# Performance work log

Hardware: AMD Instinct MI355X
Metric: run time of the kernel (lower is better)

Reference implementation:

```python
import jax, jax.numpy as jnp
import numpy as np
from jax import lax

D_VOCAB = 262
D_EMB = 128
CONV_W = 5
PAD = CONV_W // 2  # 2


def setup_inputs() -> dict:
    key = jax.random.key(0)
    k1, k2, k3, k4, k5 = jax.random.split(key, 5)
    B, W, C = 128, 256, 16
    input = jax.random.randint(k1, (B, W, C), 0, D_VOCAB, dtype=jnp.int64)
    lengths = jax.random.randint(k2, (B, W), 1, C + 1, dtype=jnp.int64)
    # torch init: Embedding weight ~ N(0,1) then *0.1
    emb_weight = jax.random.normal(k3, (D_VOCAB, D_EMB), dtype=jnp.float32) * 0.1
    fan_in = D_EMB * CONV_W
    bound = 1.0 / np.sqrt(fan_in)
    conv_w = jax.random.uniform(k4, (D_EMB, D_EMB, CONV_W), dtype=jnp.float32, minval=-bound, maxval=bound)
    conv_b = jax.random.uniform(k5, (D_EMB,), dtype=jnp.float32, minval=-bound, maxval=bound)
    return {"input": input, "lengths": lengths, "emb_weight": emb_weight,
            "conv_w": conv_w, "conv_b": conv_b}


def reference(input, lengths, emb_weight, conv_w, conv_b):
    B, W, C = input.shape
    ids = input.reshape(B * W, C)                      # [N, C]
    embed = emb_weight[ids]                            # [N, C, E] gather
    x = jnp.transpose(embed, (0, 2, 1))                # [N, E, C] (NCW)
    y = lax.conv_general_dilated(
        x, conv_w,
        window_strides=(1,), padding=[(PAD, PAD)],
        dimension_numbers=("NCH", "OIH", "NCH"))       # [N, E, C]
    y = y + conv_b[None, :, None]
    out = jnp.max(y, axis=-1)                          # max-pool over chars
    return out.reshape(B, W, -1)                       # [B, W, E]
```

## Files before the change

kernel.cpp:

```cpp
#include <hip/hip_runtime.h>
#include <hip/hip_fp16.h>

#define D_VOCAB 262
#define D_EMB   128
#define KW      5
#define NCHAR   16
#define NKO     (KW * D_EMB)

typedef _Float16 h8 __attribute__((ext_vector_type(8)));
typedef float    f8 __attribute__((ext_vector_type(8)));


__global__ __launch_bounds__(256) void transpose_w_kernel(
    const float* __restrict__ cw, float* __restrict__ Wt) {
  const int gid = blockIdx.x * 256 + threadIdx.x;
  const float val = cw[gid];
  const int o = gid / 640;
  const int r = gid - o * 640;
  const int i = r / 5;
  const int k = r - i * 5;
  Wt[(k * D_EMB + o) * D_EMB + i] = val;
}

__global__ __launch_bounds__(256) void compute_P_kernel(
    const float* __restrict__ emb, const float* __restrict__ Wt,
    _Float16* __restrict__ P) {
  const int wave = threadIdx.x >> 6;
  const int lane = threadIdx.x & 63;
  const int w = blockIdx.x * 4 + wave;
  const int v = w / 10;
  const int ko = (w - v * 10) * 64 + lane;

  const float* er = emb + v * D_EMB;
  const float4* wt = (const float4*)(Wt + ko * D_EMB);
  float acc = 0.f;
#pragma unroll 8
  for (int i4 = 0; i4 < 32; ++i4) {
    const float4 wv = wt[i4];
    acc += er[i4 * 4 + 0] * wv.x + er[i4 * 4 + 1] * wv.y +
           er[i4 * 4 + 2] * wv.z + er[i4 * 4 + 3] * wv.w;
  }
  P[v * NKO + ko] = (_Float16)acc;
}

__global__ __launch_bounds__(256) void conv_char_main_kernel(
    const int* __restrict__ ids, const _Float16* __restrict__ P,
    const float* __restrict__ bias, float* __restrict__ out) {
  const int lane = threadIdx.x & 63;
  const int wave = threadIdx.x >> 6;
  const int n_base = (blockIdx.x * 4 + wave) * 4;
  const int g4 = lane & 48;
  const int s = lane & 15;
  const int o = s * 8;
  const int n = n_base + (lane >> 4);

  const int myid = ids[n_base * NCHAR + lane];

  h8 win[5];
#pragma unroll
  for (int w = 0; w < 5; ++w) win[w] = (h8)(_Float16)0.f;
  h8 vmax = (h8)(_Float16)(-60000.f);

#pragma unroll
  for (int j = 0; j < NCHAR; ++j) {
    const int id = __shfl(myid, g4 + j);
    const _Float16* row = P + (size_t)id * NKO + o;
#pragma unroll
    for (int k = 0; k < KW; ++k) {
      const int c = j + 2 - k;
      if (c >= 0 && c < NCHAR) {
        const h8 val = *(const h8*)(row + k * D_EMB);
        win[c % 5] += val;
      }
    }
    if (j >= 2) {
      const int w = (j - 2) % 5;
      vmax = __builtin_elementwise_max(vmax, win[w]);
      win[w] = (h8)(_Float16)0.f;
    }
  }
  vmax = __builtin_elementwise_max(vmax, win[14 % 5]);
  vmax = __builtin_elementwise_max(vmax, win[15 % 5]);

  const f8 fv = __builtin_convertvector(vmax, f8);
  const f8 bv = *(const f8*)(bias + o);
  const f8 r = fv + bv;
  *(f8*)(out + (size_t)n * D_EMB + o) = r;
}

extern "C" void kernel_launch(void* const* d_in, const int* in_sizes, int n_in,
                              void* d_out, int out_size, void* d_ws, size_t ws_size,
                              hipStream_t stream) {
  const int*   input = (const int*)d_in[0];
  const float* emb   = (const float*)d_in[2];
  const float* cw    = (const float*)d_in[3];
  const float* cb    = (const float*)d_in[4];
  float* out = (float*)d_out;

  _Float16* P  = (_Float16*)d_ws;
  float*    Wt = (float*)((char*)d_ws + 335872);

  const int n_seq = in_sizes[0] / NCHAR;

  transpose_w_kernel<<<320, 256, 0, stream>>>(cw, Wt);
  compute_P_kernel<<<655, 256, 0, stream>>>(emb, Wt, P);

  const int blocks = n_seq / 16;
  conv_char_main_kernel<<<blocks, 256, 0, stream>>>(input, P, cb, out);
}
```

Measured before the change: 105.0 us.

## Stage channel-chunked projection table in LDS for the char-conv gather

The precomputed vocab×tap×channel projection table is re-laid out into 8 channel chunks of 16. Each 1024-thread block loads one chunk (about 42 KB, padded rows) into shared memory and handles 256 sequences for that chunk, so the per-character gathers hit LDS instead of global/L2. The cost is that every block reloads a chunk and the total work is split 8 ways by channel. The max is now accumulated in fp32 after half-precision window sums, and sequence bounds are checked.

```diff
diff --git a/kernel.cpp b/kernel.cpp
--- a/kernel.cpp
+++ b/kernel.cpp
@@ -5,10 +5,12 @@
 #define D_EMB   128
 #define KW      5
 #define NCHAR   16
-#define NKO     (KW * D_EMB)
-
-typedef _Float16 h8 __attribute__((ext_vector_type(8)));
-typedef float    f8 __attribute__((ext_vector_type(8)));
+#define NROW    (D_VOCAB * KW)
+#define CH      16
+#define NCHUNK  (D_EMB / CH)
+#define CHUNK_HALFS (NROW * CH)
+#define LROW2   10
+#define SEQ_PER_BLOCK 256
 
 
 __global__ __launch_bounds__(256) void transpose_w_kernel(
@@ -24,7 +26,7 @@
 
 __global__ __launch_bounds__(256) void compute_P_kernel(
     const float* __restrict__ emb, const float* __restrict__ Wt,
-    _Float16* __restrict__ P) {
+    __half* __restrict__ Pc) {
   const int wave = threadIdx.x >> 6;
   const int lane = threadIdx.x & 63;
   const int w = blockIdx.x * 4 + wave;
@@ -40,52 +42,89 @@
     acc += er[i4 * 4 + 0] * wv.x + er[i4 * 4 + 1] * wv.y +
            er[i4 * 4 + 2] * wv.z + er[i4 * 4 + 3] * wv.w;
   }
-  P[v * NKO + ko] = (_Float16)acc;
+  const int k = ko >> 7;
+  const int o = ko & 127;
+  Pc[(size_t)(o >> 4) * CHUNK_HALFS + (v * KW + k) * CH + (o & 15)] =
+      __float2half(acc);
 }
 
-__global__ __launch_bounds__(256) void conv_char_main_kernel(
-    const int* __restrict__ ids, const _Float16* __restrict__ P,
-    const float* __restrict__ bias, float* __restrict__ out) {
-  const int lane = threadIdx.x & 63;
-  const int wave = threadIdx.x >> 6;
-  const int n_base = (blockIdx.x * 4 + wave) * 4;
-  const int g4 = lane & 48;
-  const int s = lane & 15;
-  const int o = s * 8;
-  const int n = n_base + (lane >> 4);
+__global__ __launch_bounds__(1024, 8) void conv_char_main_kernel(
+    const int* __restrict__ ids, const __half* __restrict__ Pc,
+    const float* __restrict__ bias, float* __restrict__ out, int n_seq) {
+  __shared__ __half2 lds[NROW * LROW2];
 
-  const int myid = ids[n_base * NCHAR + lane];
+  const int t = threadIdx.x;
+  const int c = blockIdx.x & (NCHUNK - 1);
+  const int seqbase = (blockIdx.x >> 3) * SEQ_PER_BLOCK;
 
-  h8 win[5];
+  const int4* src = (const int4*)(Pc + (size_t)c * CHUNK_HALFS);
+  for (int t4 = t; t4 < CHUNK_HALFS / 8; t4 += 1024) {
+    const int4 v = src[t4];
+    const int row = t4 >> 1;
+    const int dst = row * LROW2 + (t4 & 1) * 4;
+    *(int2*)&lds[dst]     = make_int2(v.x, v.y);
+    *(int2*)&lds[dst + 2] = make_int2(v.z, v.w);
+  }
+  __syncthreads();
+
+  const int wave = t >> 6;
+  const int lane = t & 63;
+  const int q = lane & 3;
+  const int wseq = seqbase + wave * 16;
+  const int n = wseq + (lane >> 2);
+
+  int4 myids = make_int4(0, 0, 0, 0);
+  if (wseq + (lane >> 2) < n_seq)
+    myids = ((const int4*)(ids + (size_t)wseq * NCHAR))[lane];
+  const int ida[4] = {myids.x, myids.y, myids.z, myids.w};
+
+  const __half2 hz = __float2half2_rn(0.f);
+  __half2 win[5][2];
 #pragma unroll
-  for (int w = 0; w < 5; ++w) win[w] = (h8)(_Float16)0.f;
-  h8 vmax = (h8)(_Float16)(-60000.f);
+  for (int s = 0; s < 5; ++s) { win[s][0] = hz; win[s][1] = hz; }
+  float vmax[4] = {-1e30f, -1e30f, -1e30f, -1e30f};
 
 #pragma unroll
   for (int j = 0; j < NCHAR; ++j) {
-    const int id = __shfl(myid, g4 + j);
-    const _Float16* row = P + (size_t)id * NKO + o;
+    const int idv = __shfl(ida[j & 3], (lane & 60) + (j >> 2));
+    const __half2* rp = &lds[idv * (KW * LROW2) + q * 2];
 #pragma unroll
     for (int k = 0; k < KW; ++k) {
-      const int c = j + 2 - k;
-      if (c >= 0 && c < NCHAR) {
-        const h8 val = *(const h8*)(row + k * D_EMB);
-        win[c % 5] += val;
+      const int cc = j + 2 - k;
+      if (cc >= 0 && cc < NCHAR) {
+        const int2 rv = *(const int2*)(rp + k * LROW2);
+        const __half2 a = *(const __half2*)&rv.x;
+        const __half2 b = *(const __half2*)&rv.y;
+        __half2* ws = win[cc % 5];
+        ws[0] = __hadd2(ws[0], a);
+        ws[1] = __hadd2(ws[1], b);
       }
     }
     if (j >= 2) {
-      const int w = (j - 2) % 5;
-      vmax = __builtin_elementwise_max(vmax, win[w]);
-      win[w] = (h8)(_Float16)0.f;
+      const int s = (j - 2) % 5;
+      const float2 f0 = __half22float2(win[s][0]);
+      const float2 f1 = __half22float2(win[s][1]);
+      vmax[0] = fmaxf(vmax[0], f0.x); vmax[1] = fmaxf(vmax[1], f0.y);
+      vmax[2] = fmaxf(vmax[2], f1.x); vmax[3] = fmaxf(vmax[3], f1.y);
+      win[s][0] = hz; win[s][1] = hz;
     }
   }
-  vmax = __builtin_elementwise_max(vmax, win[14 % 5]);
-  vmax = __builtin_elementwise_max(vmax, win[15 % 5]);
+#pragma unroll
+  for (int cc = 14; cc < 16; ++cc) {
+    const int s = cc % 5;
+    const float2 f0 = __half22float2(win[s][0]);
+    const float2 f1 = __half22float2(win[s][1]);
+    vmax[0] = fmaxf(vmax[0], f0.x); vmax[1] = fmaxf(vmax[1], f0.y);
+    vmax[2] = fmaxf(vmax[2], f1.x); vmax[3] = fmaxf(vmax[3], f1.y);
+  }
 
-  const f8 fv = __builtin_convertvector(vmax, f8);
-  const f8 bv = *(const f8*)(bias + o);
-  const f8 r = fv + bv;
-  *(f8*)(out + (size_t)n * D_EMB + o) = r;
+  if (n < n_seq) {
+    const float4 bv = *(const float4*)(bias + c * CH + q * 4);
+    float4 r;
+    r.x = vmax[0] + bv.x; r.y = vmax[1] + bv.y;
+    r.z = vmax[2] + bv.z; r.w = vmax[3] + bv.w;
+    *(float4*)(out + (size_t)n * D_EMB + c * CH + q * 4) = r;
+  }
 }
 
 extern "C" void kernel_launch(void* const* d_in, const int* in_sizes, int n_in,
@@ -97,14 +136,15 @@
   const float* cb    = (const float*)d_in[4];
   float* out = (float*)d_out;
 
-  _Float16* P  = (_Float16*)d_ws;
-  float*    Wt = (float*)((char*)d_ws + 335872);
+  __half* Pc = (__half*)d_ws;
+  float*  Wt = (float*)((char*)d_ws + 335872);
 
   const int n_seq = in_sizes[0] / NCHAR;
 
   transpose_w_kernel<<<320, 256, 0, stream>>>(cw, Wt);
-  compute_P_kernel<<<655, 256, 0, stream>>>(emb, Wt, P);
+  compute_P_kernel<<<655, 256, 0, stream>>>(emb, Wt, Pc);
 
-  const int blocks = n_seq / 16;
-  conv_char_main_kernel<<<blocks, 256, 0, stream>>>(input, P, cb, out);
+  const int seq_blocks = (n_seq + SEQ_PER_BLOCK - 1) / SEQ_PER_BLOCK;
+  conv_char_main_kernel<<<seq_blocks * NCHUNK, 1024, 0, stream>>>(
+      input, Pc, cb, out, n_seq);
 }
```

After: 107.2 us. +2.2%, slower.

## Transpose conv weights to input-major layout and compute projection table per vocab row

Applied to the files above, without the earlier changes.

The conv weights are now transposed into an [i][k*E+o] layout, so each of the 640 threads in a block reads consecutive addresses when it loads one output column. Each vocab row gets one 640-thread block that stages its embedding vector in shared memory. This replaces strided per-thread float4 reads with coalesced loads across the wave. The precompute is small next to the main gather/conv kernel, so any gain is confined to that stage.

```diff
diff --git a/kernel.cpp b/kernel.cpp
--- a/kernel.cpp
+++ b/kernel.cpp
@@ -12,35 +12,31 @@
 
 
 __global__ __launch_bounds__(256) void transpose_w_kernel(
-    const float* __restrict__ cw, float* __restrict__ Wt) {
+    const float* __restrict__ cw, float* __restrict__ Wt2) {
   const int gid = blockIdx.x * 256 + threadIdx.x;
   const float val = cw[gid];
   const int o = gid / 640;
   const int r = gid - o * 640;
   const int i = r / 5;
   const int k = r - i * 5;
-  Wt[(k * D_EMB + o) * D_EMB + i] = val;
+  Wt2[i * NKO + k * D_EMB + o] = val;
 }
 
-__global__ __launch_bounds__(256) void compute_P_kernel(
-    const float* __restrict__ emb, const float* __restrict__ Wt,
-    _Float16* __restrict__ P) {
-  const int wave = threadIdx.x >> 6;
-  const int lane = threadIdx.x & 63;
-  const int w = blockIdx.x * 4 + wave;
-  const int v = w / 10;
-  const int ko = (w - v * 10) * 64 + lane;
+__global__ __launch_bounds__(640) void compute_P_kernel(
+    const float* __restrict__ emb, const float* __restrict__ Wt2,
+    __half* __restrict__ P) {
+  __shared__ float emb_s[D_EMB];
+  const int v = blockIdx.x;
+  const int t = threadIdx.x;
+  if (t < D_EMB) emb_s[t] = emb[v * D_EMB + t];
+  __syncthreads();
 
-  const float* er = emb + v * D_EMB;
-  const float4* wt = (const float4*)(Wt + ko * D_EMB);
   float acc = 0.f;
-#pragma unroll 8
-  for (int i4 = 0; i4 < 32; ++i4) {
-    const float4 wv = wt[i4];
-    acc += er[i4 * 4 + 0] * wv.x + er[i4 * 4 + 1] * wv.y +
-           er[i4 * 4 + 2] * wv.z + er[i4 * 4 + 3] * wv.w;
+#pragma unroll 16
+  for (int i = 0; i < D_EMB; ++i) {
+    acc += emb_s[i] * Wt2[i * NKO + t];
   }
-  P[v * NKO + ko] = (_Float16)acc;
+  P[v * NKO + t] = __float2half(acc);
 }
 
 __global__ __launch_bounds__(256) void conv_char_main_kernel(
@@ -97,13 +93,13 @@
   const float* cb    = (const float*)d_in[4];
   float* out = (float*)d_out;
 
-  _Float16* P  = (_Float16*)d_ws;
-  float*    Wt = (float*)((char*)d_ws + 335872);
+  _Float16* P   = (_Float16*)d_ws;
+  float*    Wt2 = (float*)((char*)d_ws + 335872);
 
   const int n_seq = in_sizes[0] / NCHAR;
 
-  transpose_w_kernel<<<320, 256, 0, stream>>>(cw, Wt);
-  compute_P_kernel<<<655, 256, 0, stream>>>(emb, Wt, P);
+  transpose_w_kernel<<<320, 256, 0, stream>>>(cw, Wt2);
+  compute_P_kernel<<<D_VOCAB, 640, 0, stream>>>(emb, Wt2, (__half*)P);
 
   const int blocks = n_seq / 16;
   conv_char_main_kernel<<<blocks, 256, 0, stream>>>(input, P, cb, out);
```

Measured after the change: 96.25 us. 1.09x faster.
